# Kernel tuning notes

Hardware: AMD Instinct MI355X
Metric: run time of the kernel (lower is better)

## Reference

```python
import jax, jax.numpy as jnp
import numpy as np

B, N, NE = 64, 512, 500
FIELD_DIM, E_DIM, HIDDEN, LATENT = 256, 64, 512, 256


def _lin_init(key, fan_in, fan_out):
    kw, kb = jax.random.split(key)
    s = 1.0 / np.sqrt(fan_in)
    W = jax.random.uniform(kw, (fan_in, fan_out), minval=-s, maxval=s, dtype=jnp.float32)
    b = jax.random.uniform(kb, (fan_out,), minval=-s, maxval=s, dtype=jnp.float32)
    return W, b


def setup_inputs() -> dict:
    key = jax.random.key(0)
    ks = jax.random.split(key, 16)
    inp = {}
    inp['field_atom_lat'] = jax.random.normal(ks[0], (B, N, FIELD_DIM), dtype=jnp.float32)
    inp['mask'] = jax.random.randint(ks[1], (B, N), 0, 2).astype(bool)
    inp['e_feat'] = jax.random.normal(ks[2], (NE, E_DIM), dtype=jnp.float32)
    # query MLP (3 layers): e_dim -> hidden -> hidden -> latent
    inp['q_w1'], inp['q_b1'] = _lin_init(ks[3], E_DIM, HIDDEN)
    inp['q_w2'], inp['q_b2'] = _lin_init(ks[4], HIDDEN, HIDDEN)
    inp['q_w3'], inp['q_b3'] = _lin_init(ks[5], HIDDEN, LATENT)
    # key MLP (3 layers): field_dim -> hidden -> hidden -> latent
    inp['k_w1'], inp['k_b1'] = _lin_init(ks[6], FIELD_DIM, HIDDEN)
    inp['k_w2'], inp['k_b2'] = _lin_init(ks[7], HIDDEN, HIDDEN)
    inp['k_w3'], inp['k_b3'] = _lin_init(ks[8], HIDDEN, LATENT)
    # value MLP (3 layers)
    inp['v_w1'], inp['v_b1'] = _lin_init(ks[9], FIELD_DIM, HIDDEN)
    inp['v_w2'], inp['v_b2'] = _lin_init(ks[10], HIDDEN, HIDDEN)
    inp['v_w3'], inp['v_b3'] = _lin_init(ks[11], HIDDEN, LATENT)
    # out MLP (2 layers): latent -> hidden -> latent
    inp['o_w1'], inp['o_b1'] = _lin_init(ks[12], LATENT, HIDDEN)
    inp['o_w2'], inp['o_b2'] = _lin_init(ks[13], HIDDEN, LATENT)
    return inp


def _mlp3(x, w1, b1, w2, b2, w3, b3):
    h = jax.nn.silu(x @ w1 + b1)
    h = jax.nn.silu(h @ w2 + b2)
    return h @ w3 + b3


def _mlp2(x, w1, b1, w2, b2):
    return jax.nn.silu(x @ w1 + b1) @ w2 + b2


def reference(field_atom_lat, mask, e_feat,
              q_w1, q_b1, q_w2, q_b2, q_w3, q_b3,
              k_w1, k_b1, k_w2, k_b2, k_w3, k_b3,
              v_w1, v_b1, v_w2, v_b2, v_w3, v_b3,
              o_w1, o_b1, o_w2, o_b2):
    latent_dim = q_w3.shape[1]
    scale = latent_dim ** (-0.5)
    q = _mlp3(e_feat, q_w1, q_b1, q_w2, q_b2, q_w3, q_b3)          # [nE, L] (shared across batch)
    k = _mlp3(field_atom_lat, k_w1, k_b1, k_w2, k_b2, k_w3, k_b3)  # [B, N, L]
    v = _mlp3(field_atom_lat, v_w1, v_b1, v_w2, v_b2, v_w3, v_b3)  # [B, N, L]
    scores = jnp.einsum('el,bnl->ben', q, k) * scale               # [B, nE, N]
    scores = jnp.where(mask[:, None, :], scores, jnp.float32(-1e9))
    attn = jax.nn.softmax(scores, axis=2)
    attn = attn * mask[:, None, :].astype(attn.dtype)              # post-softmax mask, as in torch
    out = jnp.einsum('ben,bnl->bel', attn, v)                      # [B, nE, L]
    return _mlp2(out, o_w1, o_b1, o_w2, o_b2)
```

## Files before the change

### kernel.cpp

```cpp
#include <hip/hip_runtime.h>
#include <math.h>

#define BATCH 64
#define N_ATOMS 512
#define NE 500
#define FIELD_DIM 256
#define E_DIM 64
#define HIDDEN 512
#define LATENT 256

typedef short bf16x8 __attribute__((ext_vector_type(8)));
typedef unsigned short u16x8 __attribute__((ext_vector_type(8)));
typedef unsigned short u16x4 __attribute__((ext_vector_type(4)));
typedef float f32x4 __attribute__((ext_vector_type(4)));

__device__ __forceinline__ unsigned short f2bf(float x) {
    unsigned u = __float_as_uint(x);
    unsigned r = (u + 0x7FFFu + ((u >> 16) & 1u)) >> 16;
    return (unsigned short)r;
}
__device__ __forceinline__ float bf2f(unsigned short b) {
    return __uint_as_float(((unsigned)b) << 16);
}
__device__ __forceinline__ float silu_f(float x) { return x / (1.f + __expf(-x)); }

#define GLOAD_LDS16(gptr, lptr)                                                   \
    __builtin_amdgcn_global_load_lds(                                             \
        (const __attribute__((address_space(1))) void*)(gptr),                    \
        (__attribute__((address_space(3))) void*)(lptr), 16, 0, 0)

#define QW1 0
#define QW2 32768
#define QW3 294912
#define KW1 425984
#define KW2 557056
#define KW3 819200
#define VW1 950272
#define VW2 1081344
#define VW3 1343488
#define OW1 1474560
#define OW2 1605632

template <int K, bool SILU>
__device__ __forceinline__ void mlp_layer_ip(
    const unsigned short* __restrict__ Wg, const float* __restrict__ Bg,
    unsigned short* buf, int wave, int lane, int fr, int fq)
{
    const int fb = wave * 64;
    f32x4 acc[4][4];
#pragma unroll
    for (int mf = 0; mf < 4; mf++)
#pragma unroll
        for (int nf = 0; nf < 4; nf++) acc[mf][nf] = (f32x4)0.f;

#pragma unroll
    for (int ks = 0; ks < K / 32; ks++) {
        bf16x8 wf[4], bfr[4];
#pragma unroll
        for (int mf = 0; mf < 4; mf++)
            wf[mf] = *reinterpret_cast<const bf16x8*>(
                Wg + (((long long)(wave * 4 + mf) * (K / 32) + ks) * 64 + lane) * 8);
#pragma unroll
        for (int nf = 0; nf < 4; nf++) {
            int row = nf * 16 + fr;
            bfr[nf] = *reinterpret_cast<const bf16x8*>(
                (const char*)buf + row * (K * 2) +
                ((ks * 64 + fq * 16) ^ ((row & 7) << 4)));
        }
#pragma unroll
        for (int mf = 0; mf < 4; mf++)
#pragma unroll
            for (int nf = 0; nf < 4; nf++)
                acc[mf][nf] = __builtin_amdgcn_mfma_f32_16x16x32_bf16(
                    wf[mf], bfr[nf], acc[mf][nf], 0, 0, 0);
    }
    __syncthreads();

#pragma unroll
    for (int mf = 0; mf < 4; mf++) {
        f32x4 bv = *reinterpret_cast<const f32x4*>(Bg + fb + mf * 16 + fq * 4);
#pragma unroll
        for (int nf = 0; nf < 4; nf++) {
            int row = nf * 16 + fr;
            u16x4 ov;
#pragma unroll
            for (int r = 0; r < 4; r++) {
                float x = acc[mf][nf][r] + bv[r];
                if (SILU) x = silu_f(x);
                ov[r] = f2bf(x);
            }
            *reinterpret_cast<u16x4*>(
                (char*)buf + row * 1024 +
                ((fb * 2 + mf * 32 + fq * 8) ^ ((row & 7) << 4))) = ov;
        }
    }
    __syncthreads();
}

__device__ __forceinline__ void mlp_final512(
    const unsigned short* __restrict__ Wg, const float* __restrict__ Bg,
    const unsigned short* buf, int wave, int lane, int fr, int fq,
    f32x4 (&acc)[2][4])
{
    const int fb = wave * 32;
#pragma unroll
    for (int mf = 0; mf < 2; mf++)
#pragma unroll
        for (int nf = 0; nf < 4; nf++) acc[mf][nf] = (f32x4)0.f;

#pragma unroll
    for (int ks = 0; ks < 16; ks++) {
        bf16x8 wf[2], bfr[4];
#pragma unroll
        for (int mf = 0; mf < 2; mf++)
            wf[mf] = *reinterpret_cast<const bf16x8*>(
                Wg + (((long long)(wave * 2 + mf) * 16 + ks) * 64 + lane) * 8);
#pragma unroll
        for (int nf = 0; nf < 4; nf++) {
            int row = nf * 16 + fr;
            bfr[nf] = *reinterpret_cast<const bf16x8*>(
                (const char*)buf + row * 1024 +
                ((ks * 64 + fq * 16) ^ ((row & 7) << 4)));
        }
#pragma unroll
        for (int mf = 0; mf < 2; mf++)
#pragma unroll
            for (int nf = 0; nf < 4; nf++)
                acc[mf][nf] = __builtin_amdgcn_mfma_f32_16x16x32_bf16(
                    wf[mf], bfr[nf], acc[mf][nf], 0, 0, 0);
    }
#pragma unroll
    for (int mf = 0; mf < 2; mf++) {
        f32x4 bv = *reinterpret_cast<const f32x4*>(Bg + fb + mf * 16 + fq * 4);
#pragma unroll
        for (int nf = 0; nf < 4; nf++)
#pragma unroll
            for (int r = 0; r < 4; r++) acc[mf][nf][r] += bv[r];
    }
}

__global__ __launch_bounds__(512, 2) void fused_qkv(
    const unsigned short* __restrict__ field_bf,
    const unsigned short* __restrict__ efeat_bf,
    const unsigned short* __restrict__ wt,
    const float* __restrict__ qb1, const float* __restrict__ qb2,
    const float* __restrict__ qb3, const float* __restrict__ kb1,
    const float* __restrict__ kb2, const float* __restrict__ kb3,
    const float* __restrict__ vb1, const float* __restrict__ vb2,
    const float* __restrict__ vb3,
    unsigned short* __restrict__ qbuf,
    unsigned short* __restrict__ kbuf,
    unsigned short* __restrict__ vtb)
{
    __shared__ unsigned short buf[64 * 512];
    const int t = threadIdx.x, wave = t >> 6, lane = t & 63;
    const int fr = lane & 15, fq = lane >> 4;
    const int bid = blockIdx.x;

    if (bid < 1024) {
        const int isv = bid >> 9;
        const int m0  = (bid & 511) * 64;
        const unsigned short* W1 = wt + (isv ? VW1 : KW1);
        const unsigned short* W2 = wt + (isv ? VW2 : KW2);
        const unsigned short* W3 = wt + (isv ? VW3 : KW3);
        const float* B1 = isv ? vb1 : kb1;
        const float* B2 = isv ? vb2 : kb2;
        const float* B3 = isv ? vb3 : kb3;

#pragma unroll
        for (int c = wave; c < 32; c += 8) {
            int gi  = c * 64 + lane;
            int row = gi >> 5;
            int g   = gi & 31;
            int gs  = (g & ~7) | ((g & 7) ^ (row & 7));
            GLOAD_LDS16(field_bf + (long long)(m0 + row) * 256 + gs * 8, buf + c * 512);
        }
        __syncthreads();

        mlp_layer_ip<256, true>(W1, B1, buf, wave, lane, fr, fq);
        mlp_layer_ip<512, true>(W2, B2, buf, wave, lane, fr, fq);
        f32x4 acc[2][4];
        mlp_final512(W3, B3, buf, wave, lane, fr, fq, acc);

        if (!isv) {
#pragma unroll
            for (int mf = 0; mf < 2; mf++)
#pragma unroll
                for (int nf = 0; nf < 4; nf++) {
                    int row = m0 + nf * 16 + fr;
                    u16x4 ov;
#pragma unroll
                    for (int r = 0; r < 4; r++) ov[r] = f2bf(acc[mf][nf][r]);
                    *reinterpret_cast<u16x4*>(
                        kbuf + (long long)row * 256 + wave * 32 + mf * 16 + fq * 4) = ov;
                }
        } else {
            __syncthreads();
#pragma unroll
            for (int mf = 0; mf < 2; mf++)
#pragma unroll
                for (int nf = 0; nf < 4; nf++) {
                    int row = nf * 16 + fr;
                    u16x4 ov;
#pragma unroll
                    for (int r = 0; r < 4; r++) ov[r] = f2bf(acc[mf][nf][r]);
                    *reinterpret_cast<u16x4*>(
                        (char*)buf + row * 512 +
                        ((wave * 64 + mf * 32 + fq * 8) ^ ((row & 7) << 4))) = ov;
                }
            __syncthreads();
            int l  = t >> 1;
            int nh = (t & 1) * 32;
            int b  = m0 >> 9, nb = m0 & 511;
            long long base = ((long long)b * 256 + l) * 512 + nb + nh;
#pragma unroll
            for (int q = 0; q < 4; q++) {
                u16x8 ov;
#pragma unroll
                for (int j = 0; j < 8; j++) {
                    int n = nh + q * 8 + j;
                    ov[j] = *reinterpret_cast<const unsigned short*>(
                        (const char*)buf + n * 512 + ((l * 2) ^ ((n & 7) << 4)));
                }
                *reinterpret_cast<u16x8*>(vtb + base + q * 8) = ov;
            }
        }
    } else {
        const int m0 = (bid - 1024) * 64;
        {
            int row = t >> 3;
            int g   = lane & 7;
            int gr  = m0 + row; if (gr >= NE) gr = NE - 1;
            int gs  = g ^ (row & 7);
            GLOAD_LDS16(efeat_bf + (long long)gr * 64 + gs * 8, buf + wave * 512);
        }
        __syncthreads();

        mlp_layer_ip<64, true>(wt + QW1, qb1, buf, wave, lane, fr, fq);
        mlp_layer_ip<512, true>(wt + QW2, qb2, buf, wave, lane, fr, fq);
        f32x4 acc[2][4];
        mlp_final512(wt + QW3, qb3, buf, wave, lane, fr, fq, acc);
#pragma unroll
        for (int mf = 0; mf < 2; mf++)
#pragma unroll
            for (int nf = 0; nf < 4; nf++) {
                int row = m0 + nf * 16 + fr;
                if (row < NE) {
                    u16x4 ov;
#pragma unroll
                    for (int r = 0; r < 4; r++) ov[r] = f2bf(acc[mf][nf][r]);
                    *reinterpret_cast<u16x4*>(
                        qbuf + (long long)row * 256 + wave * 32 + mf * 16 + fq * 4) = ov;
                }
            }
    }
}

__global__ __launch_bounds__(512, 2) void fused_o(
    const unsigned short* __restrict__ X,
    const unsigned short* __restrict__ wt,
    const float* __restrict__ ob1, const float* __restrict__ ob2,
    float* __restrict__ out)
{
    __shared__ unsigned short buf[64 * 512];
    const int t = threadIdx.x, wave = t >> 6, lane = t & 63;
    const int fr = lane & 15, fq = lane >> 4;
    const int m0 = blockIdx.x * 64;

#pragma unroll
    for (int c = wave; c < 32; c += 8) {
        int gi  = c * 64 + lane;
        int row = gi >> 5;
        int g   = gi & 31;
        int gs  = (g & ~7) | ((g & 7) ^ (row & 7));
        GLOAD_LDS16(X + (long long)(m0 + row) * 256 + gs * 8, buf + c * 512);
    }
    __syncthreads();

    mlp_layer_ip<256, true>(wt + OW1, ob1, buf, wave, lane, fr, fq);
    f32x4 acc[2][4];
    mlp_final512(wt + OW2, ob2, buf, wave, lane, fr, fq, acc);

#pragma unroll
    for (int mf = 0; mf < 2; mf++)
#pragma unroll
        for (int nf = 0; nf < 4; nf++) {
            int row = m0 + nf * 16 + fr;
            *reinterpret_cast<f32x4*>(
                out + (long long)row * 256 + wave * 32 + mf * 16 + fq * 4) = acc[mf][nf];
        }
}

__global__ __launch_bounds__(512, 1) void attn_fused(
    const unsigned short* __restrict__ qbuf,
    const unsigned short* __restrict__ kbuf,
    const unsigned short* __restrict__ vt,
    const int* __restrict__ mask,
    unsigned short* __restrict__ attnout)
{
    __shared__ unsigned char LDS[100352];
    unsigned short* Qs = (unsigned short*)LDS;
    unsigned short* Ks = (unsigned short*)(LDS + 32768);
    unsigned short* Ps = (unsigned short*)LDS;
    unsigned short* Vs = (unsigned short*)(LDS + 65536);
    float*          red = (float*)(LDS + 98304);

    const int id = blockIdx.x;
    const int b  = id & 63;
    const int e0 = (id >> 6) * 64;
    const int t = threadIdx.x, wave = t >> 6;
    const int lane = t & 63, fr = lane & 15, fq = lane >> 4;
    const int tr = t >> 3, tg = t & 7;

#pragma unroll
    for (int i = 0; i < 4; i++) {
        int ge = e0 + tr; if (ge >= NE) ge = NE - 1;
        int gi = tg ^ (tr & 7);
        GLOAD_LDS16(qbuf + (long long)ge * 256 + i * 64 + gi * 8,
                    Qs + i * 4096 + wave * 512);
    }
#pragma unroll
    for (int j = 0; j < 8; j++) {
        int n  = j * 64 + tr;
        int gi = tg ^ (n & 7);
        GLOAD_LDS16(kbuf + (long long)(b * 512 + n) * 256 + gi * 8,
                    Ks + j * 4096 + wave * 512);
    }
    int mk[4];
#pragma unroll
    for (int nf = 0; nf < 4; nf++) mk[nf] = mask[b * 512 + wave * 64 + nf * 16 + fr];

    f32x4 acc[4][4];
#pragma unroll
    for (int i = 0; i < 4; i++)
#pragma unroll
        for (int j = 0; j < 4; j++) acc[i][j] = (f32x4)0.f;

    __syncthreads();

    for (int ks = 0; ks < 4; ks++) {
#pragma unroll
        for (int h = 0; h < 2; h++) {
            bf16x8 af[4], bv[4];
#pragma unroll
            for (int mf = 0; mf < 4; mf++) {
                int e = mf * 16 + fr;
                int byo = ks * 8192 + e * 128 + ((h * 64 + fq * 16) ^ ((e & 7) << 4));
                af[mf] = *(const bf16x8*)((const char*)Qs + byo);
            }
#pragma unroll
            for (int nf = 0; nf < 4; nf++) {
                int n = wave * 64 + nf * 16 + fr;
                int byo = n * 128 + ((h * 64 + fq * 16) ^ ((n & 7) << 4));
                bv[nf] = *(const bf16x8*)((const char*)Ks + byo);
            }
#pragma unroll
            for (int mf = 0; mf < 4; mf++)
#pragma unroll
                for (int nf = 0; nf < 4; nf++)
                    acc[mf][nf] = __builtin_amdgcn_mfma_f32_16x16x32_bf16(
                        af[mf], bv[nf], acc[mf][nf], 0, 0, 0);
        }
        if (ks < 3) {
            __syncthreads();
#pragma unroll
            for (int j = 0; j < 8; j++) {
                int n  = j * 64 + tr;
                int gi = tg ^ (n & 7);
                GLOAD_LDS16(kbuf + (long long)(b * 512 + n) * 256 + (ks + 1) * 64 + gi * 8,
                            Ks + j * 4096 + wave * 512);
            }
            __syncthreads();
        }
    }

    const float scale = 0.0625f;
#pragma unroll
    for (int mf = 0; mf < 4; mf++)
#pragma unroll
        for (int nf = 0; nf < 4; nf++)
#pragma unroll
            for (int r = 0; r < 4; r++)
                acc[mf][nf][r] = mk[nf] ? acc[mf][nf][r] * scale : -1e9f;

    float gm[4][4];
#pragma unroll
    for (int mf = 0; mf < 4; mf++)
#pragma unroll
        for (int r = 0; r < 4; r++) {
            float m = fmaxf(fmaxf(acc[mf][0][r], acc[mf][1][r]),
                            fmaxf(acc[mf][2][r], acc[mf][3][r]));
#pragma unroll
            for (int off = 1; off < 16; off <<= 1) m = fmaxf(m, __shfl_xor(m, off, 64));
            if (fr == 0) red[(mf * 16 + fq * 4 + r) * 8 + wave] = m;
        }
    __syncthreads();
#pragma unroll
    for (int mf = 0; mf < 4; mf++)
#pragma unroll
        for (int r = 0; r < 4; r++) {
            int row = mf * 16 + fq * 4 + r;
            float4 a = *(float4*)&red[row * 8];
            float4 c = *(float4*)&red[row * 8 + 4];
            gm[mf][r] = fmaxf(fmaxf(fmaxf(a.x, a.y), fmaxf(a.z, a.w)),
                              fmaxf(fmaxf(c.x, c.y), fmaxf(c.z, c.w)));
        }
    __syncthreads();

    float inv[4][4];
#pragma unroll
    for (int mf = 0; mf < 4; mf++)
#pragma unroll
        for (int r = 0; r < 4; r++) {
            float s = 0.f;
#pragma unroll
            for (int nf = 0; nf < 4; nf++) {
                acc[mf][nf][r] = __expf(acc[mf][nf][r] - gm[mf][r]);
                s += acc[mf][nf][r];
            }
#pragma unroll
            for (int off = 1; off < 16; off <<= 1) s += __shfl_xor(s, off, 64);
            if (fr == 0) red[(mf * 16 + fq * 4 + r) * 8 + wave] = s;
        }
    __syncthreads();
#pragma unroll
    for (int mf = 0; mf < 4; mf++)
#pragma unroll
        for (int r = 0; r < 4; r++) {
            int row = mf * 16 + fq * 4 + r;
            float4 a = *(float4*)&red[row * 8];
            float4 c = *(float4*)&red[row * 8 + 4];
            inv[mf][r] = 1.f / (a.x + a.y + a.z + a.w + c.x + c.y + c.z + c.w);
        }

#pragma unroll
    for (int mf = 0; mf < 4; mf++)
#pragma unroll
        for (int nf = 0; nf < 4; nf++)
#pragma unroll
            for (int r = 0; r < 4; r++) {
                int row = mf * 16 + fq * 4 + r;
                int c   = wave * 64 + nf * 16 + fr;
                float pv = mk[nf] ? acc[mf][nf][r] * inv[mf][r] : 0.f;
                *(unsigned short*)((char*)Ps + row * 1024 + ((c * 2) ^ ((row & 7) << 4))) =
                    f2bf(pv);
            }
    __syncthreads();

    f32x4 acc2[4][2];
#pragma unroll
    for (int i = 0; i < 4; i++)
#pragma unroll
        for (int j = 0; j < 2; j++) acc2[i][j] = (f32x4)0.f;

#pragma unroll
    for (int j = 0; j < 4; j++) {
        int l  = j * 64 + tr;
        int gi = tg ^ (l & 7);
        GLOAD_LDS16(vt + (long long)(b * 256 + l) * 512 + gi * 8,
                    Vs + j * 4096 + wave * 512);
    }
    __syncthreads();

    for (int ks = 0; ks < 8; ks++) {
#pragma unroll
        for (int h = 0; h < 2; h++) {
            bf16x8 af[4], bv[2];
#pragma unroll
            for (int mf = 0; mf < 4; mf++) {
                int e = mf * 16 + fr;
                int byo = e * 1024 + ((ks * 128 + h * 64 + fq * 16) ^ ((e & 7) << 4));
                af[mf] = *(const bf16x8*)((const char*)Ps + byo);
            }
#pragma unroll
            for (int nf = 0; nf < 2; nf++) {
                int l = wave * 32 + nf * 16 + fr;
                int byo = l * 128 + ((h * 64 + fq * 16) ^ ((l & 7) << 4));
                bv[nf] = *(const bf16x8*)((const char*)Vs + byo);
            }
#pragma unroll
            for (int mf = 0; mf < 4; mf++)
#pragma unroll
                for (int nf = 0; nf < 2; nf++)
                    acc2[mf][nf] = __builtin_amdgcn_mfma_f32_16x16x32_bf16(
                        af[mf], bv[nf], acc2[mf][nf], 0, 0, 0);
        }
        if (ks < 7) {
            __syncthreads();
#pragma unroll
            for (int j = 0; j < 4; j++) {
                int l  = j * 64 + tr;
                int gi = tg ^ (l & 7);
                GLOAD_LDS16(vt + (long long)(b * 256 + l) * 512 + (ks + 1) * 64 + gi * 8,
                            Vs + j * 4096 + wave * 512);
            }
            __syncthreads();
        }
    }

#pragma unroll
    for (int mf = 0; mf < 4; mf++)
#pragma unroll
        for (int nf = 0; nf < 2; nf++)
#pragma unroll
            for (int r = 0; r < 4; r++) {
                int e = e0 + mf * 16 + fq * 4 + r;
                if (e < NE) {
                    int l = wave * 32 + nf * 16 + fr;
                    attnout[((long long)b * NE + e) * 256 + l] = f2bf(acc2[mf][nf][r]);
                }
            }
}

__global__ __launch_bounds__(256) void f32_to_bf16(
    const float* __restrict__ in, unsigned short* __restrict__ out, long long n8)
{
    long long i      = (long long)blockIdx.x * 256 + threadIdx.x;
    long long stride = (long long)gridDim.x * 256;
    for (; i < n8; i += stride) {
        const float4* p = reinterpret_cast<const float4*>(in + i * 8);
        float4 a = p[0], b = p[1];
        u16x8 o;
        o[0] = f2bf(a.x); o[1] = f2bf(a.y); o[2] = f2bf(a.z); o[3] = f2bf(a.w);
        o[4] = f2bf(b.x); o[5] = f2bf(b.y); o[6] = f2bf(b.z); o[7] = f2bf(b.w);
        *reinterpret_cast<u16x8*>(out + i * 8) = o;
    }
}

__global__ __launch_bounds__(256) void wt_pack(
    const float* w0, const float* w1, const float* w2, const float* w3,
    const float* w4, const float* w5, const float* w6, const float* w7,
    const float* w8, const float* w9, const float* w10, unsigned short* dst)
{
    const int Kd[11] = {64, 512, 512, 256, 512, 512, 256, 512, 512, 256, 512};
    const int Nd[11] = {512, 512, 256, 512, 512, 256, 512, 512, 256, 512, 256};
    const long long Od[11] = {QW1, QW2, QW3, KW1, KW2, KW3, VW1, VW2, VW3, OW1, OW2};
    const int z = blockIdx.z;
    const float* src = z == 0 ? w0 : z == 1 ? w1 : z == 2 ? w2 : z == 3 ? w3 :
                       z == 4 ? w4 : z == 5 ? w5 : z == 6 ? w6 : z == 7 ? w7 :
                       z == 8 ? w8 : z == 9 ? w9 : w10;
    const int K = Kd[z], N = Nd[z];
    const int k0 = blockIdx.y * 64, n0 = blockIdx.x * 64;
    if (k0 >= K || n0 >= N) return;

    __shared__ float tf[64][65];
    const int t = threadIdx.x;
    {
        const int r = t >> 2;
        const int c0 = (t & 3) * 16;
        const float* srow = src + (long long)(k0 + r) * N + n0 + c0;
#pragma unroll
        for (int q = 0; q < 4; q++) {
            float4 xv = *reinterpret_cast<const float4*>(srow + q * 4);
            tf[r][c0 + q * 4 + 0] = xv.x;
            tf[r][c0 + q * 4 + 1] = xv.y;
            tf[r][c0 + q * 4 + 2] = xv.z;
            tf[r][c0 + q * 4 + 3] = xv.w;
        }
    }
    __syncthreads();

#pragma unroll
    for (int it = 0; it < 2; it++) {
        int wi = t + it * 256;
        int nc = wi & 63;
        int k8 = wi >> 6;
        int kg = k0 + k8 * 8;
        int ks = kg >> 5;
        int fq = (kg >> 3) & 3;
        int f16 = (n0 + nc) >> 4;
        int fr  = nc & 15;
        u16x8 ov;
#pragma unroll
        for (int e = 0; e < 8; e++) ov[e] = f2bf(tf[k8 * 8 + e][nc]);
        long long off = Od[z] +
            (((long long)f16 * (K / 32) + ks) * 64 + fq * 16 + fr) * 8;
        *reinterpret_cast<u16x8*>(dst + off) = ov;
    }
}

extern "C" void kernel_launch(void* const* d_in, const int* in_sizes, int n_in,
                              void* d_out, int out_size, void* d_ws, size_t ws_size,
                              hipStream_t stream)
{
    const float* field = (const float*)d_in[0];
    const int*   mask  = (const int*)d_in[1];
    const float* efeat = (const float*)d_in[2];
    const float* q_w1 = (const float*)d_in[3];  const float* q_b1 = (const float*)d_in[4];
    const float* q_w2 = (const float*)d_in[5];  const float* q_b2 = (const float*)d_in[6];
    const float* q_w3 = (const float*)d_in[7];  const float* q_b3 = (const float*)d_in[8];
    const float* k_w1 = (const float*)d_in[9];  const float* k_b1 = (const float*)d_in[10];
    const float* k_w2 = (const float*)d_in[11]; const float* k_b2 = (const float*)d_in[12];
    const float* k_w3 = (const float*)d_in[13]; const float* k_b3 = (const float*)d_in[14];
    const float* v_w1 = (const float*)d_in[15]; const float* v_b1 = (const float*)d_in[16];
    const float* v_w2 = (const float*)d_in[17]; const float* v_b2 = (const float*)d_in[18];
    const float* v_w3 = (const float*)d_in[19]; const float* v_b3 = (const float*)d_in[20];
    const float* o_w1 = (const float*)d_in[21]; const float* o_b1 = (const float*)d_in[22];
    const float* o_w2 = (const float*)d_in[23]; const float* o_b2 = (const float*)d_in[24];

    unsigned short* ws = (unsigned short*)d_ws;
    unsigned short* field_bf = ws;
    unsigned short* efeat_bf = ws + 8388608;
    unsigned short* wt       = ws + 8420608;
    unsigned short* qbuf     = ws + 10157312;
    unsigned short* kbuf     = ws + 10285312;
    unsigned short* vtb      = ws + 18673920;
    unsigned short* attnout  = ws + 27062528;

    f32_to_bf16<<<dim3(2048), dim3(256), 0, stream>>>(field, field_bf, 1048576);
    f32_to_bf16<<<dim3(16),   dim3(256), 0, stream>>>(efeat, efeat_bf, 4000);
    wt_pack<<<dim3(8, 8, 11), dim3(256), 0, stream>>>(
        q_w1, q_w2, q_w3, k_w1, k_w2, k_w3, v_w1, v_w2, v_w3, o_w1, o_w2, wt);

    fused_qkv<<<dim3(1032), dim3(512), 0, stream>>>(
        field_bf, efeat_bf, wt, q_b1, q_b2, q_b3, k_b1, k_b2, k_b3,
        v_b1, v_b2, v_b3, qbuf, kbuf, vtb);

    attn_fused<<<dim3(512), dim3(512), 0, stream>>>(qbuf, kbuf, vtb, mask, attnout);

    fused_o<<<dim3(500), dim3(512), 0, stream>>>(
        attnout, wt, o_b1, o_b2, (float*)d_out);
}
```

Baseline: 240.4 us.

## Fuse output MLP into attention kernel and prefetch MLP weight fragments

The output MLP is moved into the attention kernel epilogue: each block writes its attention result tile to LDS and runs both output layers there, which removes the attnout global round-trip and the separate fused_o launch. The MLP GEMM loops now prefetch the next k-step's weight fragments one step ahead (double-buffered registers) and raise wave priority around the MFMA bursts. The risks are higher register pressure in the attention kernel, which runs at one block per CU, and the O-MLP work being spread over only 512 blocks instead of 500 independent blocks at two per CU.

```diff
diff --git a/kernel.cpp b/kernel.cpp
--- a/kernel.cpp
+++ b/kernel.cpp
@@ -46,20 +46,31 @@
     const unsigned short* __restrict__ Wg, const float* __restrict__ Bg,
     unsigned short* buf, int wave, int lane, int fr, int fq)
 {
+    constexpr int NS = K / 32;
     const int fb = wave * 64;
+    const unsigned short* wp = Wg + (long long)(wave * 4) * NS * 512 + lane * 8;
+
     f32x4 acc[4][4];
 #pragma unroll
     for (int mf = 0; mf < 4; mf++)
 #pragma unroll
         for (int nf = 0; nf < 4; nf++) acc[mf][nf] = (f32x4)0.f;
 
-#pragma unroll
-    for (int ks = 0; ks < K / 32; ks++) {
-        bf16x8 wf[4], bfr[4];
-#pragma unroll
-        for (int mf = 0; mf < 4; mf++)
-            wf[mf] = *reinterpret_cast<const bf16x8*>(
-                Wg + (((long long)(wave * 4 + mf) * (K / 32) + ks) * 64 + lane) * 8);
+    bf16x8 wfA[4];
+#pragma unroll
+    for (int mf = 0; mf < 4; mf++)
+        wfA[mf] = *reinterpret_cast<const bf16x8*>(wp + (long long)mf * NS * 512);
+
+#pragma unroll
+    for (int ks = 0; ks < NS; ks++) {
+        bf16x8 wfB[4];
+        if (ks + 1 < NS) {
+#pragma unroll
+            for (int mf = 0; mf < 4; mf++)
+                wfB[mf] = *reinterpret_cast<const bf16x8*>(
+                    wp + ((long long)mf * NS + (ks + 1)) * 512);
+        }
+        bf16x8 bfr[4];
 #pragma unroll
         for (int nf = 0; nf < 4; nf++) {
             int row = nf * 16 + fr;
@@ -67,12 +78,18 @@
                 (const char*)buf + row * (K * 2) +
                 ((ks * 64 + fq * 16) ^ ((row & 7) << 4)));
         }
+        __builtin_amdgcn_s_setprio(1);
 #pragma unroll
         for (int mf = 0; mf < 4; mf++)
 #pragma unroll
             for (int nf = 0; nf < 4; nf++)
                 acc[mf][nf] = __builtin_amdgcn_mfma_f32_16x16x32_bf16(
-                    wf[mf], bfr[nf], acc[mf][nf], 0, 0, 0);
+                    wfA[mf], bfr[nf], acc[mf][nf], 0, 0, 0);
+        __builtin_amdgcn_s_setprio(0);
+        if (ks + 1 < NS) {
+#pragma unroll
+            for (int mf = 0; mf < 4; mf++) wfA[mf] = wfB[mf];
+        }
     }
     __syncthreads();
 
@@ -91,6 +108,79 @@
             }
             *reinterpret_cast<u16x4*>(
                 (char*)buf + row * 1024 +
+                ((fb * 2 + mf * 32 + fq * 8) ^ ((row & 7) << 4))) = ov;
+        }
+    }
+    __syncthreads();
+}
+
+template <int K, bool SILU>
+__device__ __forceinline__ void mlp_layer_io(
+    const unsigned short* __restrict__ Wg, const float* __restrict__ Bg,
+    const unsigned short* inb, unsigned short* outb, int wave, int lane,
+    int fr, int fq)
+{
+    constexpr int NS = K / 32;
+    const int fb = wave * 64;
+    const unsigned short* wp = Wg + (long long)(wave * 4) * NS * 512 + lane * 8;
+
+    f32x4 acc[4][4];
+#pragma unroll
+    for (int mf = 0; mf < 4; mf++)
+#pragma unroll
+        for (int nf = 0; nf < 4; nf++) acc[mf][nf] = (f32x4)0.f;
+
+    bf16x8 wfA[4];
+#pragma unroll
+    for (int mf = 0; mf < 4; mf++)
+        wfA[mf] = *reinterpret_cast<const bf16x8*>(wp + (long long)mf * NS * 512);
+
+#pragma unroll
+    for (int ks = 0; ks < NS; ks++) {
+        bf16x8 wfB[4];
+        if (ks + 1 < NS) {
+#pragma unroll
+            for (int mf = 0; mf < 4; mf++)
+                wfB[mf] = *reinterpret_cast<const bf16x8*>(
+                    wp + ((long long)mf * NS + (ks + 1)) * 512);
+        }
+        bf16x8 bfr[4];
+#pragma unroll
+        for (int nf = 0; nf < 4; nf++) {
+            int row = nf * 16 + fr;
+            bfr[nf] = *reinterpret_cast<const bf16x8*>(
+                (const char*)inb + row * (K * 2) +
+                ((ks * 64 + fq * 16) ^ ((row & 7) << 4)));
+        }
+        __builtin_amdgcn_s_setprio(1);
+#pragma unroll
+        for (int mf = 0; mf < 4; mf++)
+#pragma unroll
+            for (int nf = 0; nf < 4; nf++)
+                acc[mf][nf] = __builtin_amdgcn_mfma_f32_16x16x32_bf16(
+                    wfA[mf], bfr[nf], acc[mf][nf], 0, 0, 0);
+        __builtin_amdgcn_s_setprio(0);
+        if (ks + 1 < NS) {
+#pragma unroll
+            for (int mf = 0; mf < 4; mf++) wfA[mf] = wfB[mf];
+        }
+    }
+
+#pragma unroll
+    for (int mf = 0; mf < 4; mf++) {
+        f32x4 bv = *reinterpret_cast<const f32x4*>(Bg + fb + mf * 16 + fq * 4);
+#pragma unroll
+        for (int nf = 0; nf < 4; nf++) {
+            int row = nf * 16 + fr;
+            u16x4 ov;
+#pragma unroll
+            for (int r = 0; r < 4; r++) {
+                float x = acc[mf][nf][r] + bv[r];
+                if (SILU) x = silu_f(x);
+                ov[r] = f2bf(x);
+            }
+            *reinterpret_cast<u16x4*>(
+                (char*)outb + row * 1024 +
                 ((fb * 2 + mf * 32 + fq * 8) ^ ((row & 7) << 4))) = ov;
         }
     }
@@ -103,18 +193,27 @@
     f32x4 (&acc)[2][4])
 {
     const int fb = wave * 32;
+    const unsigned short* wp = Wg + (long long)(wave * 2) * 16 * 512 + lane * 8;
 #pragma unroll
     for (int mf = 0; mf < 2; mf++)
 #pragma unroll
         for (int nf = 0; nf < 4; nf++) acc[mf][nf] = (f32x4)0.f;
 
+    bf16x8 wfA[2];
+#pragma unroll
+    for (int mf = 0; mf < 2; mf++)
+        wfA[mf] = *reinterpret_cast<const bf16x8*>(wp + (long long)mf * 16 * 512);
+
 #pragma unroll
     for (int ks = 0; ks < 16; ks++) {
-        bf16x8 wf[2], bfr[4];
-#pragma unroll
-        for (int mf = 0; mf < 2; mf++)
-            wf[mf] = *reinterpret_cast<const bf16x8*>(
-                Wg + (((long long)(wave * 2 + mf) * 16 + ks) * 64 + lane) * 8);
+        bf16x8 wfB[2];
+        if (ks + 1 < 16) {
+#pragma unroll
+            for (int mf = 0; mf < 2; mf++)
+                wfB[mf] = *reinterpret_cast<const bf16x8*>(
+                    wp + ((long long)mf * 16 + (ks + 1)) * 512);
+        }
+        bf16x8 bfr[4];
 #pragma unroll
         for (int nf = 0; nf < 4; nf++) {
             int row = nf * 16 + fr;
@@ -122,12 +221,18 @@
                 (const char*)buf + row * 1024 +
                 ((ks * 64 + fq * 16) ^ ((row & 7) << 4)));
         }
+        __builtin_amdgcn_s_setprio(1);
 #pragma unroll
         for (int mf = 0; mf < 2; mf++)
 #pragma unroll
             for (int nf = 0; nf < 4; nf++)
                 acc[mf][nf] = __builtin_amdgcn_mfma_f32_16x16x32_bf16(
-                    wf[mf], bfr[nf], acc[mf][nf], 0, 0, 0);
+                    wfA[mf], bfr[nf], acc[mf][nf], 0, 0, 0);
+        __builtin_amdgcn_s_setprio(0);
+        if (ks + 1 < 16) {
+#pragma unroll
+            for (int mf = 0; mf < 2; mf++) wfA[mf] = wfB[mf];
+        }
     }
 #pragma unroll
     for (int mf = 0; mf < 2; mf++) {
@@ -256,47 +361,14 @@
     }
 }
 
-__global__ __launch_bounds__(512, 2) void fused_o(
-    const unsigned short* __restrict__ X,
-    const unsigned short* __restrict__ wt,
-    const float* __restrict__ ob1, const float* __restrict__ ob2,
-    float* __restrict__ out)
-{
-    __shared__ unsigned short buf[64 * 512];
-    const int t = threadIdx.x, wave = t >> 6, lane = t & 63;
-    const int fr = lane & 15, fq = lane >> 4;
-    const int m0 = blockIdx.x * 64;
-
-#pragma unroll
-    for (int c = wave; c < 32; c += 8) {
-        int gi  = c * 64 + lane;
-        int row = gi >> 5;
-        int g   = gi & 31;
-        int gs  = (g & ~7) | ((g & 7) ^ (row & 7));
-        GLOAD_LDS16(X + (long long)(m0 + row) * 256 + gs * 8, buf + c * 512);
-    }
-    __syncthreads();
-
-    mlp_layer_ip<256, true>(wt + OW1, ob1, buf, wave, lane, fr, fq);
-    f32x4 acc[2][4];
-    mlp_final512(wt + OW2, ob2, buf, wave, lane, fr, fq, acc);
-
-#pragma unroll
-    for (int mf = 0; mf < 2; mf++)
-#pragma unroll
-        for (int nf = 0; nf < 4; nf++) {
-            int row = m0 + nf * 16 + fr;
-            *reinterpret_cast<f32x4*>(
-                out + (long long)row * 256 + wave * 32 + mf * 16 + fq * 4) = acc[mf][nf];
-        }
-}
-
 __global__ __launch_bounds__(512, 1) void attn_fused(
     const unsigned short* __restrict__ qbuf,
     const unsigned short* __restrict__ kbuf,
     const unsigned short* __restrict__ vt,
     const int* __restrict__ mask,
-    unsigned short* __restrict__ attnout)
+    const unsigned short* __restrict__ wt,
+    const float* __restrict__ ob1, const float* __restrict__ ob2,
+    float* __restrict__ out)
 {
     __shared__ unsigned char LDS[100352];
     unsigned short* Qs = (unsigned short*)LDS;
@@ -304,6 +376,8 @@
     unsigned short* Ps = (unsigned short*)LDS;
     unsigned short* Vs = (unsigned short*)(LDS + 65536);
     float*          red = (float*)(LDS + 98304);
+    unsigned short* oin  = (unsigned short*)(LDS + 65536);
+    unsigned short* obuf = (unsigned short*)LDS;
 
     const int id = blockIdx.x;
     const int b  = id & 63;
@@ -498,18 +572,35 @@
         }
     }
 
+    __syncthreads();
 #pragma unroll
     for (int mf = 0; mf < 4; mf++)
 #pragma unroll
         for (int nf = 0; nf < 2; nf++)
 #pragma unroll
             for (int r = 0; r < 4; r++) {
-                int e = e0 + mf * 16 + fq * 4 + r;
-                if (e < NE) {
-                    int l = wave * 32 + nf * 16 + fr;
-                    attnout[((long long)b * NE + e) * 256 + l] = f2bf(acc2[mf][nf][r]);
-                }
-            }
+                int row = mf * 16 + fq * 4 + r;
+                int col = wave * 32 + nf * 16 + fr;
+                *(unsigned short*)((char*)oin + row * 512 +
+                                   ((col * 2) ^ ((row & 7) << 4))) =
+                    f2bf(acc2[mf][nf][r]);
+            }
+    __syncthreads();
+
+    mlp_layer_io<256, true>(wt + OW1, ob1, oin, obuf, wave, lane, fr, fq);
+    f32x4 oacc[2][4];
+    mlp_final512(wt + OW2, ob2, obuf, wave, lane, fr, fq, oacc);
+
+#pragma unroll
+    for (int mf = 0; mf < 2; mf++)
+#pragma unroll
+        for (int nf = 0; nf < 4; nf++) {
+            int e = e0 + nf * 16 + fr;
+            if (e < NE)
+                *reinterpret_cast<f32x4*>(
+                    out + ((long long)b * NE + e) * 256 + wave * 32 + mf * 16 + fq * 4) =
+                    oacc[mf][nf];
+        }
 }
 
 __global__ __launch_bounds__(256) void f32_to_bf16(
@@ -605,7 +696,6 @@
     unsigned short* qbuf     = ws + 10157312;
     unsigned short* kbuf     = ws + 10285312;
     unsigned short* vtb      = ws + 18673920;
-    unsigned short* attnout  = ws + 27062528;
 
     f32_to_bf16<<<dim3(2048), dim3(256), 0, stream>>>(field, field_bf, 1048576);
     f32_to_bf16<<<dim3(16),   dim3(256), 0, stream>>>(efeat, efeat_bf, 4000);
@@ -616,8 +706,6 @@
         field_bf, efeat_bf, wt, q_b1, q_b2, q_b3, k_b1, k_b2, k_b3,
         v_b1, v_b2, v_b3, qbuf, kbuf, vtb);
 
-    attn_fused<<<dim3(512), dim3(512), 0, stream>>>(qbuf, kbuf, vtb, mask, attnout);
-
-    fused_o<<<dim3(500), dim3(512), 0, stream>>>(
-        attnout, wt, o_b1, o_b2, (float*)d_out);
-}
+    attn_fused<<<dim3(512), dim3(512), 0, stream>>>(
+        qbuf, kbuf, vtb, mask, wt, o_b1, o_b2, (float*)d_out);
+}
```

Result: faster. 210.6 us (median of 2 runs) (-12.4%).
